# Kernel tuning notes

Measured on AMD Instinct MI355X. Metric: run time of the kernel, lower is better.

Reference implementation:

```python
import jax, jax.numpy as jnp
import numpy as np

S, B, H = 2048, 1, 1024
N_HEADS = 16
HEAD_DIM = H // N_HEADS
E, K, F = 8, 2, 2048  # experts, top_k, ffn_hidden
EPS = 1e-5


def layernorm(x, w, b):
    mu = jnp.mean(x, axis=-1, keepdims=True)
    var = jnp.mean(jnp.square(x - mu), axis=-1, keepdims=True)
    return (x - mu) * jax.lax.rsqrt(var + EPS) * w + b


def setup_inputs() -> dict:
    key = jax.random.key(0)
    ks = jax.random.split(key, 8)
    std = 0.02
    return {
        "x": jax.random.normal(ks[0], (S, B, H), dtype=jnp.float32),
        "ln1_w": jnp.ones((H,), jnp.float32),
        "ln1_b": jnp.zeros((H,), jnp.float32),
        "in_proj_w": jax.random.normal(ks[1], (3 * H, H), jnp.float32) * std,
        "in_proj_b": jnp.zeros((3 * H,), jnp.float32),
        "out_proj_w": jax.random.normal(ks[2], (H, H), jnp.float32) * std,
        "out_proj_b": jnp.zeros((H,), jnp.float32),
        "ln2_w": jnp.ones((H,), jnp.float32),
        "ln2_b": jnp.zeros((H,), jnp.float32),
        "router_w": jax.random.normal(ks[3], (E, H), jnp.float32) * std,
        "w1": jax.random.normal(ks[4], (E, H, F), jnp.float32) * std,
        "w2": jax.random.normal(ks[5], (E, F, H), jnp.float32) * std,
    }


def reference(x, ln1_w, ln1_b, in_proj_w, in_proj_b, out_proj_w, out_proj_b,
              ln2_w, ln2_b, router_w, w1, w2):
    s, b, h = x.shape
    # ---- causal self-attention (nn.MultiheadAttention math) ----
    hn = layernorm(x, ln1_w, ln1_b)
    qkv = hn @ in_proj_w.T + in_proj_b          # [S,B,3H]
    q, k, v = jnp.split(qkv, 3, axis=-1)
    q = q.reshape(s, b, N_HEADS, HEAD_DIM)
    k = k.reshape(s, b, N_HEADS, HEAD_DIM)
    v = v.reshape(s, b, N_HEADS, HEAD_DIM)
    scores = jnp.einsum('sbnd,tbnd->bnst', q, k) / np.sqrt(HEAD_DIM)
    causal = jnp.tril(jnp.ones((s, s), bool))
    scores = jnp.where(causal[None, None], scores, -jnp.inf)
    probs = jax.nn.softmax(scores, axis=-1)
    attn = jnp.einsum('bnst,tbnd->sbnd', probs, v).reshape(s, b, h)
    attn = attn @ out_proj_w.T + out_proj_b
    x1 = x + attn
    # ---- dMoE FFN: router softmax -> top-k gates -> expert GELU MLP ----
    hn2 = layernorm(x1, ln2_w, ln2_b).reshape(s * b, h)   # tokens [T,H]
    logits = hn2 @ router_w.T                              # [T,E]
    rp = jax.nn.softmax(logits, axis=-1)
    topw, topi = jax.lax.top_k(rp, K)                      # [T,K]
    gates = jnp.sum(jax.nn.one_hot(topi, E, dtype=hn2.dtype) * topw[..., None], axis=1)  # [T,E]
    hmid = jax.nn.gelu(jnp.einsum('th,ehf->tef', hn2, w1), approximate=False)  # [T,E,F]
    y = jnp.einsum('tef,efh->th', hmid * gates[:, :, None], w2)                # [T,H]
    return x1 + y.reshape(s, b, h)
```

## Files before the change

### kernel.cpp

```cpp
#include <hip/hip_runtime.h>

#define SL 2048
#define HID 1024
#define NHEAD 16
#define HD 64
#define NEXP 8
#define FF 2048
#define MAXTILE 40
#define MAXROWS (MAXTILE * 128)
#define CPAD 32

typedef short bf16x8 __attribute__((ext_vector_type(8)));
typedef float f32x4 __attribute__((ext_vector_type(4)));

__device__ __forceinline__ unsigned short f2bf(float f) {
  unsigned u = __builtin_bit_cast(unsigned, f);
  u += 0x7fffu + ((u >> 16) & 1u);
  return (unsigned short)(u >> 16);
}

__device__ __forceinline__ void gload16(const void* g, void* l) {
  __builtin_amdgcn_global_load_lds((const __attribute__((address_space(1))) void*)g,
                                   (__attribute__((address_space(3))) void*)l,
                                   16, 0, 0);
}

__device__ __forceinline__ void xcd_remap(int& bx, int& by) {
  const int nx = gridDim.x;
  const int nwg = nx * gridDim.y;
  const int L = by * nx + bx;
  const int per = nwg >> 3;
  const int Lp = (L & 7) * per + (L >> 3);
  bx = Lp % nx;
  by = Lp / nx;
}

template <int MODE>
__global__ __launch_bounds__(256) void gemm_bt(
    const unsigned short* __restrict__ A, const unsigned short* __restrict__ Bt,
    int M, int N, int Kstride, int Kloop,
    const float* __restrict__ bias,
    float* __restrict__ outf,
    unsigned short* __restrict__ q_out, unsigned short* __restrict__ k_out,
    unsigned short* __restrict__ vt_out)
{
  __shared__ unsigned short Asm[2][128 * 32];
  __shared__ unsigned short Bsm[2][128 * 32];
  int bx = blockIdx.x, by = blockIdx.y;
  xcd_remap(bx, by);
  const int tid = threadIdx.x;
  const int wave = tid >> 6;
  const int lane = tid & 63;
  const int m0 = by * 128;
  const int n0 = bx * 128;
  const int koff = blockIdx.z * Kloop;
  const int wm = (wave >> 1) * 64;
  const int wn = (wave & 1) * 64;

  f32x4 acc[4][4] = {};

  const int srow = tid >> 2;
  const int skoff = (tid & 3) * 8;
  const unsigned short* Ag = A + (size_t)(m0 + srow) * Kstride + koff + skoff;
  const unsigned short* Bg = Bt + (size_t)(n0 + srow) * Kstride + koff + skoff;

  const int la = lane & 15;
  const int lk = (lane >> 4) * 8;

  auto stage = [&](int buf, int k0) {
    gload16(Ag + k0, &Asm[buf][wave * 512]);
    gload16(Ag + (size_t)64 * Kstride + k0, &Asm[buf][2048 + wave * 512]);
    gload16(Bg + k0, &Bsm[buf][wave * 512]);
    gload16(Bg + (size_t)64 * Kstride + k0, &Bsm[buf][2048 + wave * 512]);
  };

  stage(0, 0);
  __syncthreads();
  int cur = 0;
  for (int k0 = 0; k0 < Kloop; k0 += 32) {
    if (k0 + 32 < Kloop) stage(cur ^ 1, k0 + 32);
    bf16x8 af[4], bfr[4];
#pragma unroll
    for (int mt = 0; mt < 4; mt++)
      af[mt] = *reinterpret_cast<const bf16x8*>(&Asm[cur][(wm + mt * 16 + la) * 32 + lk]);
#pragma unroll
    for (int nt = 0; nt < 4; nt++)
      bfr[nt] = *reinterpret_cast<const bf16x8*>(&Bsm[cur][(wn + nt * 16 + la) * 32 + lk]);
#pragma unroll
    for (int mt = 0; mt < 4; mt++)
#pragma unroll
      for (int nt = 0; nt < 4; nt++)
        acc[mt][nt] = __builtin_amdgcn_mfma_f32_16x16x32_bf16(af[mt], bfr[nt], acc[mt][nt], 0, 0, 0);
    __syncthreads();
    cur ^= 1;
  }

  const int lg = lane >> 4;
#pragma unroll
  for (int mt = 0; mt < 4; mt++) {
#pragma unroll
    for (int nt = 0; nt < 4; nt++) {
#pragma unroll
      for (int r = 0; r < 4; r++) {
        const int row = m0 + wm + mt * 16 + lg * 4 + r;
        const int col = n0 + wn + nt * 16 + la;
        float v = acc[mt][nt][r];
        if (MODE == 0) {
          v += bias[col];
          const int hh = (col & 1023) >> 6;
          const int dd = col & 63;
          const unsigned short bv = f2bf(v);
          if (col < 1024)
            q_out[(size_t)hh * SL * HD + (size_t)row * HD + dd] = bv;
          else if (col < 2048)
            k_out[(size_t)hh * SL * HD + (size_t)row * HD + dd] = bv;
          else
            vt_out[(size_t)hh * HD * SL + (size_t)dd * SL + row] = bv;
        } else {
          outf[(size_t)blockIdx.z * SL * HID + (size_t)row * HID + col] = v;
        }
      }
    }
  }
}

__global__ __launch_bounds__(256) void gemm_moe1(
    const unsigned short* __restrict__ A, const unsigned short* __restrict__ w1t,
    const int* __restrict__ perm, const float* __restrict__ gateg,
    const int* __restrict__ texp, const int* __restrict__ trow,
    unsigned short* __restrict__ hmidg)
{
  int bx = blockIdx.x, by = blockIdx.y;
  xcd_remap(bx, by);
  const int e = texp[by];
  if (e < 0) return;
  const int row0 = trow[by];
  __shared__ unsigned short Asm[2][128 * 32];
  __shared__ unsigned short Bsm[2][128 * 32];
  const int tid = threadIdx.x;
  const int wave = tid >> 6;
  const int lane = tid & 63;
  const int n0 = bx * 128;
  const int wm = (wave >> 1) * 64;
  const int wn = (wave & 1) * 64;
  f32x4 acc[4][4] = {};
  const int srow = tid >> 2;
  const int skoff = (tid & 3) * 8;
  const int p0 = perm[row0 + srow];
  const int p1 = perm[row0 + 64 + srow];
  const unsigned short* Ag0 = A + (size_t)(p0 < 0 ? 0 : (p0 >> 1)) * HID + skoff;
  const unsigned short* Ag1 = A + (size_t)(p1 < 0 ? 0 : (p1 >> 1)) * HID + skoff;
  const unsigned short* Bg = w1t + (size_t)e * HID * FF + (size_t)(n0 + srow) * HID + skoff;
  const int la = lane & 15;
  const int lk = (lane >> 4) * 8;

  auto stage = [&](int buf, int k0) {
    gload16(Ag0 + k0, &Asm[buf][wave * 512]);
    gload16(Ag1 + k0, &Asm[buf][2048 + wave * 512]);
    gload16(Bg + k0, &Bsm[buf][wave * 512]);
    gload16(Bg + (size_t)64 * HID + k0, &Bsm[buf][2048 + wave * 512]);
  };

  stage(0, 0);
  __syncthreads();
  int cur = 0;
  for (int k0 = 0; k0 < HID; k0 += 32) {
    if (k0 + 32 < HID) stage(cur ^ 1, k0 + 32);
    bf16x8 af[4], bfr[4];
#pragma unroll
    for (int mt = 0; mt < 4; mt++)
      af[mt] = *reinterpret_cast<const bf16x8*>(&Asm[cur][(wm + mt * 16 + la) * 32 + lk]);
#pragma unroll
    for (int nt = 0; nt < 4; nt++)
      bfr[nt] = *reinterpret_cast<const bf16x8*>(&Bsm[cur][(wn + nt * 16 + la) * 32 + lk]);
#pragma unroll
    for (int mt = 0; mt < 4; mt++)
#pragma unroll
      for (int nt = 0; nt < 4; nt++)
        acc[mt][nt] = __builtin_amdgcn_mfma_f32_16x16x32_bf16(af[mt], bfr[nt], acc[mt][nt], 0, 0, 0);
    __syncthreads();
    cur ^= 1;
  }

  const int lg = lane >> 4;
#pragma unroll
  for (int mt = 0; mt < 4; mt++) {
    float gr[4];
#pragma unroll
    for (int r = 0; r < 4; r++) gr[r] = gateg[row0 + wm + mt * 16 + lg * 4 + r];
#pragma unroll
    for (int nt = 0; nt < 4; nt++) {
#pragma unroll
      for (int r = 0; r < 4; r++) {
        const int grow = row0 + wm + mt * 16 + lg * 4 + r;
        const int col = n0 + wn + nt * 16 + la;
        const float v = acc[mt][nt][r];
        const float g = 0.5f * v * (1.0f + erff(v * 0.70710678118f));
        hmidg[(size_t)grow * FF + col] = f2bf(g * gr[r]);
      }
    }
  }
}

__global__ __launch_bounds__(256) void gemm_moe2(
    const unsigned short* __restrict__ A, const unsigned short* __restrict__ w2t,
    const int* __restrict__ perm,
    const int* __restrict__ texp, const int* __restrict__ trow,
    float* __restrict__ ybuf)
{
  int bx = blockIdx.x, by = blockIdx.y;
  xcd_remap(bx, by);
  const int e = texp[by];
  if (e < 0) return;
  const int row0 = trow[by];
  __shared__ unsigned short Asm[2][128 * 32];
  __shared__ unsigned short Bsm[2][128 * 32];
  const int tid = threadIdx.x;
  const int wave = tid >> 6;
  const int lane = tid & 63;
  const int n0 = bx * 128;
  const int koff = blockIdx.z * (FF / 2);
  const int wm = (wave >> 1) * 64;
  const int wn = (wave & 1) * 64;
  f32x4 acc[4][4] = {};
  const int srow = tid >> 2;
  const int skoff = (tid & 3) * 8;
  const unsigned short* Ag = A + (size_t)(row0 + srow) * FF + koff + skoff;
  const unsigned short* Bg = w2t + (size_t)e * FF * HID + (size_t)(n0 + srow) * FF + koff + skoff;
  const int la = lane & 15;
  const int lk = (lane >> 4) * 8;

  auto stage = [&](int buf, int k0) {
    gload16(Ag + k0, &Asm[buf][wave * 512]);
    gload16(Ag + (size_t)64 * FF + k0, &Asm[buf][2048 + wave * 512]);
    gload16(Bg + k0, &Bsm[buf][wave * 512]);
    gload16(Bg + (size_t)64 * FF + k0, &Bsm[buf][2048 + wave * 512]);
  };

  stage(0, 0);
  __syncthreads();
  int cur = 0;
  for (int k0 = 0; k0 < FF / 2; k0 += 32) {
    if (k0 + 32 < FF / 2) stage(cur ^ 1, k0 + 32);
    bf16x8 af[4], bfr[4];
#pragma unroll
    for (int mt = 0; mt < 4; mt++)
      af[mt] = *reinterpret_cast<const bf16x8*>(&Asm[cur][(wm + mt * 16 + la) * 32 + lk]);
#pragma unroll
    for (int nt = 0; nt < 4; nt++)
      bfr[nt] = *reinterpret_cast<const bf16x8*>(&Bsm[cur][(wn + nt * 16 + la) * 32 + lk]);
#pragma unroll
    for (int mt = 0; mt < 4; mt++)
#pragma unroll
      for (int nt = 0; nt < 4; nt++)
        acc[mt][nt] = __builtin_amdgcn_mfma_f32_16x16x32_bf16(af[mt], bfr[nt], acc[mt][nt], 0, 0, 0);
    __syncthreads();
    cur ^= 1;
  }

  const int lg = lane >> 4;
#pragma unroll
  for (int mt = 0; mt < 4; mt++) {
    int pr[4];
#pragma unroll
    for (int r = 0; r < 4; r++) pr[r] = perm[row0 + wm + mt * 16 + lg * 4 + r];
#pragma unroll
    for (int nt = 0; nt < 4; nt++) {
#pragma unroll
      for (int r = 0; r < 4; r++) {
        const int p = pr[r];
        if (p >= 0) {
          const int col = n0 + wn + nt * 16 + la;
          ybuf[(size_t)(blockIdx.z * 2 + (p & 1)) * SL * HID + (size_t)(p >> 1) * HID + col] =
              acc[mt][nt][r];
        }
      }
    }
  }
}

__global__ __launch_bounds__(256) void ln_kernel(
    const float* __restrict__ x, const float* __restrict__ w, const float* __restrict__ b,
    unsigned short* __restrict__ ob, float* __restrict__ of)
{
  const int row = blockIdx.x;
  const int tid = threadIdx.x;
  const float4 v = *reinterpret_cast<const float4*>(&x[(size_t)row * HID + tid * 4]);
  float s = v.x + v.y + v.z + v.w;
  float q = v.x * v.x + v.y * v.y + v.z * v.z + v.w * v.w;
  for (int off = 32; off > 0; off >>= 1) {
    s += __shfl_down(s, off);
    q += __shfl_down(q, off);
  }
  __shared__ float ps[4], pq[4];
  const int wave = tid >> 6, lane = tid & 63;
  if (lane == 0) { ps[wave] = s; pq[wave] = q; }
  __syncthreads();
  s = ps[0] + ps[1] + ps[2] + ps[3];
  q = pq[0] + pq[1] + pq[2] + pq[3];
  const float mu = s * (1.0f / HID);
  const float inv = rsqrtf(q * (1.0f / HID) - mu * mu + 1e-5f);
  const int i = tid * 4;
  const float4 wv = *reinterpret_cast<const float4*>(&w[i]);
  const float4 bv = *reinterpret_cast<const float4*>(&b[i]);
  const float o0 = (v.x - mu) * inv * wv.x + bv.x;
  const float o1 = (v.y - mu) * inv * wv.y + bv.y;
  const float o2 = (v.z - mu) * inv * wv.z + bv.z;
  const float o3 = (v.w - mu) * inv * wv.w + bv.w;
  ushort4 u; u.x = f2bf(o0); u.y = f2bf(o1); u.z = f2bf(o2); u.w = f2bf(o3);
  *reinterpret_cast<ushort4*>(&ob[(size_t)row * HID + i]) = u;
  if (of) {
    float4 o; o.x = o0; o.y = o1; o.z = o2; o.w = o3;
    *reinterpret_cast<float4*>(&of[(size_t)row * HID + i]) = o;
  }
}

__global__ __launch_bounds__(256) void transpose_bf16(
    const float* __restrict__ in, unsigned short* __restrict__ out, int R, int C)
{
  __shared__ float tile[32][33];
  const size_t base = (size_t)blockIdx.z * R * C;
  const int r0 = blockIdx.y * 32, c0 = blockIdx.x * 32;
  const int tx = threadIdx.x & 31, ty = threadIdx.x >> 5;
#pragma unroll
  for (int j = 0; j < 4; j++)
    tile[ty + j * 8][tx] = in[base + (size_t)(r0 + ty + j * 8) * C + c0 + tx];
  __syncthreads();
#pragma unroll
  for (int j = 0; j < 4; j++)
    out[base + (size_t)(c0 + ty + j * 8) * R + r0 + tx] = f2bf(tile[tx][ty + j * 8]);
}

__global__ __launch_bounds__(256) void conv_bf16(
    const float4* __restrict__ in, ushort4* __restrict__ out, int n4)
{
  const int i = blockIdx.x * 256 + threadIdx.x;
  if (i < n4) {
    const float4 v = in[i];
    ushort4 u; u.x = f2bf(v.x); u.y = f2bf(v.y); u.z = f2bf(v.z); u.w = f2bf(v.w);
    out[i] = u;
  }
}

__global__ __launch_bounds__(256) void router_kernel(
    const float* __restrict__ hn2f, const float* __restrict__ rw,
    int* __restrict__ ti, float* __restrict__ tg, int* __restrict__ cnt)
{
  __shared__ float wlds[NEXP * HID];
  __shared__ int lcnt[NEXP];
  const int tid = threadIdx.x;
#pragma unroll
  for (int i = 0; i < 8; i++)
    *reinterpret_cast<float4*>(&wlds[i * 1024 + tid * 4]) =
        *reinterpret_cast<const float4*>(&rw[i * 1024 + tid * 4]);
  if (tid < NEXP) lcnt[tid] = 0;
  __syncthreads();

  const int wave = tid >> 6, lane = tid & 63;
#pragma unroll 1
  for (int k = 0; k < 4; k++) {
    const int t = blockIdx.x * 16 + wave * 4 + k;
    float4 xr[4];
#pragma unroll
    for (int c = 0; c < 4; c++)
      xr[c] = *reinterpret_cast<const float4*>(&hn2f[(size_t)t * HID + c * 256 + lane * 4]);
    float p[NEXP];
#pragma unroll
    for (int e = 0; e < NEXP; e++) {
      float s = 0.f;
#pragma unroll
      for (int c = 0; c < 4; c++) {
        const float4 wv = *reinterpret_cast<const float4*>(&wlds[e * 1024 + c * 256 + lane * 4]);
        s += xr[c].x * wv.x + xr[c].y * wv.y + xr[c].z * wv.z + xr[c].w * wv.w;
      }
      s += __shfl_xor(s, 32);
      s += __shfl_xor(s, 16);
      s += __shfl_xor(s, 8);
      s += __shfl_xor(s, 4);
      s += __shfl_xor(s, 2);
      s += __shfl_xor(s, 1);
      p[e] = s;
    }
    if (lane == 0) {
      float mx = p[0];
#pragma unroll
      for (int e = 1; e < NEXP; e++) mx = fmaxf(mx, p[e]);
      float Z = 0.f;
#pragma unroll
      for (int e = 0; e < NEXP; e++) { p[e] = expf(p[e] - mx); Z += p[e]; }
      const float invZ = 1.f / Z;
      int i1 = 0;
#pragma unroll
      for (int e = 1; e < NEXP; e++) if (p[e] > p[i1]) i1 = e;
      int i2 = (i1 == 0) ? 1 : 0;
#pragma unroll
      for (int e = 0; e < NEXP; e++) if (e != i1 && p[e] > p[i2]) i2 = e;
      ti[2 * t] = i1; ti[2 * t + 1] = i2;
      tg[2 * t] = p[i1] * invZ; tg[2 * t + 1] = p[i2] * invZ;
      atomicAdd(&lcnt[i1], 1);
      atomicAdd(&lcnt[i2], 1);
    }
  }
  __syncthreads();
  if (tid < NEXP && lcnt[tid] > 0) atomicAdd(&cnt[tid * CPAD], lcnt[tid]);
}

__global__ void scan_kernel(const int* __restrict__ cnt, int* __restrict__ poff,
                            int* __restrict__ texp, int* __restrict__ trow)
{
  if (threadIdx.x == 0 && blockIdx.x == 0) {
    int off = 0, nt = 0;
    for (int e = 0; e < NEXP; e++) {
      poff[e] = off;
      const int c = cnt[e * CPAD];
      const int ntl = (c + 127) >> 7;
      for (int i = 0; i < ntl; i++) { texp[nt] = e; trow[nt] = off + i * 128; nt++; }
      off += ntl * 128;
    }
    for (int i = nt; i < MAXTILE; i++) { texp[i] = -1; trow[i] = 0; }
  }
}

__global__ __launch_bounds__(256) void build_kernel(
    const int* __restrict__ ti, const float* __restrict__ tg,
    const int* __restrict__ poff, int* __restrict__ fill,
    int* __restrict__ perm, float* __restrict__ gateg)
{
  __shared__ int lcnt[NEXP], lbase[NEXP];
  const int tid = threadIdx.x;
  if (tid < NEXP) lcnt[tid] = 0;
  __syncthreads();
  const int t = blockIdx.x * 256 + tid;
  int e0 = ti[2 * t], e1 = ti[2 * t + 1];
  int l0 = atomicAdd(&lcnt[e0], 1);
  int l1 = atomicAdd(&lcnt[e1], 1);
  __syncthreads();
  if (tid < NEXP) lbase[tid] = (lcnt[tid] > 0) ? atomicAdd(&fill[tid * CPAD], lcnt[tid]) : 0;
  __syncthreads();
  int pos0 = poff[e0] + lbase[e0] + l0;
  int pos1 = poff[e1] + lbase[e1] + l1;
  perm[pos0] = 2 * t;
  gateg[pos0] = tg[2 * t];
  perm[pos1] = 2 * t + 1;
  gateg[pos1] = tg[2 * t + 1];
}

__global__ __launch_bounds__(256) void combine_x1(
    const float4* __restrict__ x, const float* __restrict__ bias,
    const float4* __restrict__ p0, const float4* __restrict__ p1,
    float4* __restrict__ x1)
{
  const int i = blockIdx.x * 256 + threadIdx.x;
  const int col = (i * 4) & (HID - 1);
  const float4 bv = *reinterpret_cast<const float4*>(&bias[col]);
  const float4 a = x[i], b = p0[i], c = p1[i];
  float4 o;
  o.x = a.x + bv.x + b.x + c.x;
  o.y = a.y + bv.y + b.y + c.y;
  o.z = a.z + bv.z + b.z + c.z;
  o.w = a.w + bv.w + b.w + c.w;
  x1[i] = o;
}

__global__ __launch_bounds__(256) void final_add(
    const float4* __restrict__ x1, const float4* __restrict__ y0,
    const float4* __restrict__ y1, const float4* __restrict__ y2,
    const float4* __restrict__ y3, float4* __restrict__ out)
{
  const int i = blockIdx.x * 256 + threadIdx.x;
  const float4 a = x1[i], b = y0[i], c = y1[i], d = y2[i], e = y3[i];
  float4 o;
  o.x = a.x + b.x + c.x + d.x + e.x;
  o.y = a.y + b.y + c.y + d.y + e.y;
  o.z = a.z + b.z + c.z + d.z + e.z;
  o.w = a.w + b.w + c.w + d.w + e.w;
  out[i] = o;
}

#define SC2 0.1803368801111204f
__global__ __launch_bounds__(512) void attn_kernel(
    const unsigned short* __restrict__ qb, const unsigned short* __restrict__ kb,
    const unsigned short* __restrict__ vtb, unsigned short* __restrict__ attn)
{
  const int h = blockIdx.y;
  const int tid = threadIdx.x;
  const int wave = tid >> 6, lane = tid & 63;
  const int grp = wave >> 2;
  const int w4 = wave & 3;
  const int la = lane & 15, lg = lane >> 4;
  const int la7 = la & 7;
  __shared__ unsigned short Kt[2][2][64 * 64];
  __shared__ unsigned short Vt[2][2][64 * 64];
  __shared__ unsigned short plds[8 * 16 * 64];
  const unsigned short* qh = qb + (size_t)h * SL * HD;
  const unsigned short* kh = kb + (size_t)h * SL * HD;
  const unsigned short* vh = vtb + (size_t)h * HD * SL;

  const int sr_lo = w4 * 8 + (lane >> 3);
  const int ss = lane & 7;

  auto stageKV = [&](int t, int buf) {
    const int kvb = t * 64;
#pragma unroll
    for (int j = 0; j < 2; j++) {
      const int row = j * 32 + sr_lo;
      const int s = ss ^ (row & 7);
      gload16(kh + (size_t)(kvb + row) * HD + s * 8, &Kt[grp][buf][j * 2048 + w4 * 512]);
      gload16(vh + (size_t)row * SL + kvb + s * 8, &Vt[grp][buf][j * 2048 + w4 * 512]);
    }
  };

  for (int half = 0; half < 2; half++) {
    const int qt = half ? (31 - blockIdx.x) : blockIdx.x;
    const int m0 = qt * 64 + w4 * 16;
    const int T = qt + 1;
    const int S = (T + 1) >> 1;

    bf16x8 aq0 = *reinterpret_cast<const bf16x8*>(&qh[(size_t)(m0 + la) * HD + lg * 8]);
    bf16x8 aq1 = *reinterpret_cast<const bf16x8*>(&qh[(size_t)(m0 + la) * HD + 32 + lg * 8]);

    f32x4 oacc[4] = {};
    float mrow[4] = {-1e30f, -1e30f, -1e30f, -1e30f};
    float lrow[4] = {0.f, 0.f, 0.f, 0.f};

    if (grp < T) stageKV(grp, 0);
    __syncthreads();
    int cur = 0;

    for (int s = 0; s < S; s++) {
      const int tmy = 2 * s + grp;
      if (tmy + 2 < T) stageKV(tmy + 2, cur ^ 1);
      if (tmy < T) {
        const int kv0 = tmy * 64;
        const unsigned short* Kb = Kt[grp][cur];
        const unsigned short* Vb = Vt[grp][cur];

        f32x4 sac[4] = {};
#pragma unroll
        for (int nt = 0; nt < 4; nt++) {
          const int row = nt * 16 + la;
          bf16x8 b0 = *reinterpret_cast<const bf16x8*>(&Kb[row * 64 + ((lg ^ la7) << 3)]);
          bf16x8 b1 = *reinterpret_cast<const bf16x8*>(&Kb[row * 64 + (((4 + lg) ^ la7) << 3)]);
          sac[nt] = __builtin_amdgcn_mfma_f32_16x16x32_bf16(aq0, b0, sac[nt], 0, 0, 0);
          sac[nt] = __builtin_amdgcn_mfma_f32_16x16x32_bf16(aq1, b1, sac[nt], 0, 0, 0);
        }
        float sv[4][4];
        const bool diag = (tmy == qt);
#pragma unroll
        for (int nt = 0; nt < 4; nt++)
#pragma unroll
          for (int r = 0; r < 4; r++) {
            float xs = sac[nt][r] * SC2;
            if (diag && (kv0 + nt * 16 + la) > (m0 + lg * 4 + r)) xs = -1e30f;
            sv[nt][r] = xs;
          }
        float alpha[4];
#pragma unroll
        for (int r = 0; r < 4; r++) {
          float tm = fmaxf(fmaxf(sv[0][r], sv[1][r]), fmaxf(sv[2][r], sv[3][r]));
          tm = fmaxf(tm, __shfl_xor(tm, 1));
          tm = fmaxf(tm, __shfl_xor(tm, 2));
          tm = fmaxf(tm, __shfl_xor(tm, 4));
          tm = fmaxf(tm, __shfl_xor(tm, 8));
          const float mn = fmaxf(mrow[r], tm);
          alpha[r] = exp2f(mrow[r] - mn);
          float rs = 0.f;
#pragma unroll
          for (int nt = 0; nt < 4; nt++) {
            const float pe = exp2f(sv[nt][r] - mn);
            sv[nt][r] = pe;
            rs += pe;
          }
          rs += __shfl_xor(rs, 1);
          rs += __shfl_xor(rs, 2);
          rs += __shfl_xor(rs, 4);
          rs += __shfl_xor(rs, 8);
          lrow[r] = lrow[r] * alpha[r] + rs;
          mrow[r] = mn;
        }
#pragma unroll
        for (int dt = 0; dt < 4; dt++)
#pragma unroll
          for (int r = 0; r < 4; r++) oacc[dt][r] *= alpha[r];

#pragma unroll
        for (int nt = 0; nt < 4; nt++)
#pragma unroll
          for (int r = 0; r < 4; r++) {
            const int row = lg * 4 + r;
            const int slot = nt * 2 + (la >> 3);
            plds[wave * 1024 + row * 64 + ((slot ^ (row & 7)) << 3) + la7] = f2bf(sv[nt][r]);
          }
        asm volatile("s_waitcnt lgkmcnt(0)" ::: "memory");
        bf16x8 pa0 = *reinterpret_cast<const bf16x8*>(&plds[wave * 1024 + la * 64 + ((lg ^ la7) << 3)]);
        bf16x8 pa1 = *reinterpret_cast<const bf16x8*>(&plds[wave * 1024 + la * 64 + (((4 + lg) ^ la7) << 3)]);
#pragma unroll
        for (int dt = 0; dt < 4; dt++) {
          const int row = dt * 16 + la;
          bf16x8 v0 = *reinterpret_cast<const bf16x8*>(&Vb[row * 64 + ((lg ^ la7) << 3)]);
          bf16x8 v1 = *reinterpret_cast<const bf16x8*>(&Vb[row * 64 + (((4 + lg) ^ la7) << 3)]);
          oacc[dt] = __builtin_amdgcn_mfma_f32_16x16x32_bf16(pa0, v0, oacc[dt], 0, 0, 0);
          oacc[dt] = __builtin_amdgcn_mfma_f32_16x16x32_bf16(pa1, v1, oacc[dt], 0, 0, 0);
        }
      }
      __syncthreads();
      cur ^= 1;
    }

    float* xb = (float*)&Kt[0][0][0];
    float* mlb = (float*)&Vt[0][0][0];
    if (grp == 1) {
#pragma unroll
      for (int dt = 0; dt < 4; dt++)
#pragma unroll
        for (int r = 0; r < 4; r++)
          xb[w4 * 1024 + (lg * 4 + r) * 64 + dt * 16 + la] = oacc[dt][r];
      if (la == 0) {
#pragma unroll
        for (int r = 0; r < 4; r++) {
          mlb[w4 * 32 + (lg * 4 + r) * 2] = mrow[r];
          mlb[w4 * 32 + (lg * 4 + r) * 2 + 1] = lrow[r];
        }
      }
    }
    __syncthreads();
    if (grp == 0) {
#pragma unroll
      for (int r = 0; r < 4; r++) {
        const int row = lg * 4 + r;
        const float m1 = mlb[w4 * 32 + row * 2];
        const float l1 = mlb[w4 * 32 + row * 2 + 1];
        const float mm = fmaxf(mrow[r], m1);
        const float a0 = exp2f(mrow[r] - mm);
        const float a1 = exp2f(m1 - mm);
        const float linv = 1.0f / (lrow[r] * a0 + l1 * a1);
#pragma unroll
        for (int dt = 0; dt < 4; dt++) {
          const float o1 = xb[w4 * 1024 + row * 64 + dt * 16 + la];
          const float o = (oacc[dt][r] * a0 + o1 * a1) * linv;
          attn[(size_t)(m0 + row) * HID + h * HD + dt * 16 + la] = f2bf(o);
        }
      }
    }
    __syncthreads();
  }
}

extern "C" void kernel_launch(void* const* d_in, const int* in_sizes, int n_in,
                              void* d_out, int out_size, void* d_ws, size_t ws_size,
                              hipStream_t stream)
{
  const float* x          = (const float*)d_in[0];
  const float* ln1_w      = (const float*)d_in[1];
  const float* ln1_b      = (const float*)d_in[2];
  const float* in_proj_w  = (const float*)d_in[3];
  const float* in_proj_b  = (const float*)d_in[4];
  const float* out_proj_w = (const float*)d_in[5];
  const float* out_proj_b = (const float*)d_in[6];
  const float* ln2_w      = (const float*)d_in[7];
  const float* ln2_b      = (const float*)d_in[8];
  const float* router_w   = (const float*)d_in[9];
  const float* w1         = (const float*)d_in[10];
  const float* w2         = (const float*)d_in[11];
  float* out = (float*)d_out;

  char* ws = (char*)d_ws;
  size_t off = 0;
  auto alloc = [&](size_t bytes) -> void* {
    void* p = ws + off;
    off += (bytes + 255) & ~(size_t)255;
    return p;
  };
  unsigned short* hn_b   = (unsigned short*)alloc((size_t)SL * HID * 2);
  unsigned short* ipw_b  = (unsigned short*)alloc((size_t)3 * HID * HID * 2);
  unsigned short* opw_b  = (unsigned short*)alloc((size_t)HID * HID * 2);
  unsigned short* qb     = (unsigned short*)alloc((size_t)SL * HID * 2);
  unsigned short* kb     = (unsigned short*)alloc((size_t)SL * HID * 2);
  unsigned short* vtb    = (unsigned short*)alloc((size_t)SL * HID * 2);
  unsigned short* attn_b = (unsigned short*)alloc((size_t)SL * HID * 2);
  float*          x1     = (float*)alloc((size_t)SL * HID * 4);
  float*          pbuf   = (float*)alloc((size_t)2 * SL * HID * 4);
  unsigned short* hn2_b  = (unsigned short*)alloc((size_t)SL * HID * 2);
  float*          hn2_f  = (float*)alloc((size_t)SL * HID * 4);
  unsigned short* w1t    = (unsigned short*)alloc((size_t)NEXP * HID * FF * 2);
  unsigned short* w2t    = (unsigned short*)alloc((size_t)NEXP * HID * FF * 2);
  unsigned short* hmidg  = (unsigned short*)alloc((size_t)MAXROWS * FF * 2);
  float*          ybuf   = (float*)alloc((size_t)4 * SL * HID * 4);
  int*            ti     = (int*)alloc((size_t)SL * 2 * 4);
  float*          tg     = (float*)alloc((size_t)SL * 2 * 4);
  int*            perm   = (int*)alloc((size_t)MAXROWS * 4);
  float*          gateg  = (float*)alloc((size_t)MAXROWS * 4);
  int*            cnt    = (int*)alloc(NEXP * CPAD * 4);
  int*            fill   = (int*)alloc(NEXP * CPAD * 4);
  int*            poff   = (int*)alloc(64 * 4);
  int*            texp   = (int*)alloc(64 * 4);
  int*            trow   = (int*)alloc(64 * 4);

  const dim3 blk(256);

  hipMemsetAsync(cnt, 0, NEXP * CPAD * 4, stream);
  hipMemsetAsync(fill, 0, NEXP * CPAD * 4, stream);
  hipMemsetAsync(perm, 0xFF, (size_t)MAXROWS * 4, stream);
  hipMemsetAsync(gateg, 0, (size_t)MAXROWS * 4, stream);

  conv_bf16<<<(3 * HID * HID / 4 + 255) / 256, blk, 0, stream>>>(
      (const float4*)in_proj_w, (ushort4*)ipw_b, 3 * HID * HID / 4);
  conv_bf16<<<(HID * HID / 4 + 255) / 256, blk, 0, stream>>>(
      (const float4*)out_proj_w, (ushort4*)opw_b, HID * HID / 4);
  transpose_bf16<<<dim3(FF / 32, HID / 32, NEXP), blk, 0, stream>>>(w1, w1t, HID, FF);
  transpose_bf16<<<dim3(HID / 32, FF / 32, NEXP), blk, 0, stream>>>(w2, w2t, FF, HID);

  ln_kernel<<<SL, blk, 0, stream>>>(x, ln1_w, ln1_b, hn_b, nullptr);

  gemm_bt<0><<<dim3(3 * HID / 128, SL / 128), blk, 0, stream>>>(
      hn_b, ipw_b, SL, 3 * HID, HID, HID,
      in_proj_b, nullptr, qb, kb, vtb);

  attn_kernel<<<dim3(16, NHEAD), dim3(512), 0, stream>>>(qb, kb, vtb, attn_b);

  gemm_bt<2><<<dim3(HID / 128, SL / 128, 2), blk, 0, stream>>>(
      attn_b, opw_b, SL, HID, HID, HID / 2,
      nullptr, pbuf, nullptr, nullptr, nullptr);
  combine_x1<<<SL * HID / 1024, blk, 0, stream>>>(
      (const float4*)x, out_proj_b, (const float4*)pbuf,
      (const float4*)(pbuf + (size_t)SL * HID), (float4*)x1);

  ln_kernel<<<SL, blk, 0, stream>>>(x1, ln2_w, ln2_b, hn2_b, hn2_f);

  router_kernel<<<SL / 16, blk, 0, stream>>>(hn2_f, router_w, ti, tg, cnt);
  scan_kernel<<<1, 64, 0, stream>>>(cnt, poff, texp, trow);
  build_kernel<<<SL / 256, blk, 0, stream>>>(ti, tg, poff, fill, perm, gateg);

  gemm_moe1<<<dim3(FF / 128, MAXTILE), blk, 0, stream>>>(
      hn2_b, w1t, perm, gateg, texp, trow, hmidg);
  gemm_moe2<<<dim3(HID / 128, MAXTILE, 2), blk, 0, stream>>>(
      hmidg, w2t, perm, texp, trow, ybuf);

  final_add<<<SL * HID / 1024, blk, 0, stream>>>(
      (const float4*)x1, (const float4*)ybuf,
      (const float4*)(ybuf + (size_t)SL * HID),
      (const float4*)(ybuf + (size_t)2 * SL * HID),
      (const float4*)(ybuf + (size_t)3 * SL * HID),
      (float4*)out);
}
```

Before: 284.5 us.

## Transpose attention MFMA operands for per-lane softmax rows and widen weight transpose

The attention kernel swaps the MFMA A/B operands so each lane holds one query row. The softmax max and sum then need only two cross-lane shuffles, and the output rescale is skipped when no row max increases in the wave. P is packed to bf16 pairs with v_cvt_pk_bf16_f32 into a padded LDS layout, and the output is written as ushort4. Separately, the weight transpose kernel moves to 64x64 tiles with float4 loads and ushort4 stores, cutting memory transactions in the per-call weight conversion at the cost of more LDS per block.

```diff
diff --git a/kernel.cpp b/kernel.cpp
--- a/kernel.cpp
+++ b/kernel.cpp
@@ -12,6 +12,7 @@
 
 typedef short bf16x8 __attribute__((ext_vector_type(8)));
 typedef float f32x4 __attribute__((ext_vector_type(4)));
+typedef unsigned u32x4 __attribute__((ext_vector_type(4)));
 
 __device__ __forceinline__ unsigned short f2bf(float f) {
   unsigned u = __builtin_bit_cast(unsigned, f);
@@ -318,17 +319,27 @@
 __global__ __launch_bounds__(256) void transpose_bf16(
     const float* __restrict__ in, unsigned short* __restrict__ out, int R, int C)
 {
-  __shared__ float tile[32][33];
+  __shared__ float t[64][65];
   const size_t base = (size_t)blockIdx.z * R * C;
-  const int r0 = blockIdx.y * 32, c0 = blockIdx.x * 32;
-  const int tx = threadIdx.x & 31, ty = threadIdx.x >> 5;
-#pragma unroll
-  for (int j = 0; j < 4; j++)
-    tile[ty + j * 8][tx] = in[base + (size_t)(r0 + ty + j * 8) * C + c0 + tx];
-  __syncthreads();
-#pragma unroll
-  for (int j = 0; j < 4; j++)
-    out[base + (size_t)(c0 + ty + j * 8) * R + r0 + tx] = f2bf(tile[tx][ty + j * 8]);
+  const int r0 = blockIdx.y * 64, c0 = blockIdx.x * 64;
+  const int tid = threadIdx.x;
+#pragma unroll
+  for (int it = 0; it < 4; it++) {
+    const int idx = it * 256 + tid;
+    const int r = idx >> 4, c4 = (idx & 15) * 4;
+    const float4 v = *reinterpret_cast<const float4*>(&in[base + (size_t)(r0 + r) * C + c0 + c4]);
+    t[r][c4] = v.x; t[r][c4 + 1] = v.y; t[r][c4 + 2] = v.z; t[r][c4 + 3] = v.w;
+  }
+  __syncthreads();
+#pragma unroll
+  for (int it = 0; it < 4; it++) {
+    const int idx = it * 256 + tid;
+    const int c = idx >> 4, r4 = (idx & 15) * 4;
+    ushort4 u;
+    u.x = f2bf(t[r4][c]); u.y = f2bf(t[r4 + 1][c]);
+    u.z = f2bf(t[r4 + 2][c]); u.w = f2bf(t[r4 + 3][c]);
+    *reinterpret_cast<ushort4*>(&out[base + (size_t)(c0 + c) * R + r0 + r4]) = u;
+  }
 }
 
 __global__ __launch_bounds__(256) void conv_bf16(
@@ -478,6 +489,7 @@
 }
 
 #define SC2 0.1803368801111204f
+#define PPITCH 20
 __global__ __launch_bounds__(512) void attn_kernel(
     const unsigned short* __restrict__ qb, const unsigned short* __restrict__ kb,
     const unsigned short* __restrict__ vtb, unsigned short* __restrict__ attn)
@@ -491,10 +503,11 @@
   const int la7 = la & 7;
   __shared__ unsigned short Kt[2][2][64 * 64];
   __shared__ unsigned short Vt[2][2][64 * 64];
-  __shared__ unsigned short plds[8 * 16 * 64];
+  __shared__ unsigned plds[8 * 32 * PPITCH];
   const unsigned short* qh = qb + (size_t)h * SL * HD;
   const unsigned short* kh = kb + (size_t)h * SL * HD;
   const unsigned short* vh = vtb + (size_t)h * HD * SL;
+  unsigned* pu = &plds[wave * 32 * PPITCH];
 
   const int sr_lo = w4 * 8 + (lane >> 3);
   const int ss = lane & 7;
@@ -515,13 +528,13 @@
     const int m0 = qt * 64 + w4 * 16;
     const int T = qt + 1;
     const int S = (T + 1) >> 1;
+    const int q = m0 + la;
 
     bf16x8 aq0 = *reinterpret_cast<const bf16x8*>(&qh[(size_t)(m0 + la) * HD + lg * 8]);
     bf16x8 aq1 = *reinterpret_cast<const bf16x8*>(&qh[(size_t)(m0 + la) * HD + 32 + lg * 8]);
 
     f32x4 oacc[4] = {};
-    float mrow[4] = {-1e30f, -1e30f, -1e30f, -1e30f};
-    float lrow[4] = {0.f, 0.f, 0.f, 0.f};
+    float mrun = -1e30f, lrun = 0.f;
 
     if (grp < T) stageKV(grp, 0);
     __syncthreads();
@@ -541,8 +554,8 @@
           const int row = nt * 16 + la;
           bf16x8 b0 = *reinterpret_cast<const bf16x8*>(&Kb[row * 64 + ((lg ^ la7) << 3)]);
           bf16x8 b1 = *reinterpret_cast<const bf16x8*>(&Kb[row * 64 + (((4 + lg) ^ la7) << 3)]);
-          sac[nt] = __builtin_amdgcn_mfma_f32_16x16x32_bf16(aq0, b0, sac[nt], 0, 0, 0);
-          sac[nt] = __builtin_amdgcn_mfma_f32_16x16x32_bf16(aq1, b1, sac[nt], 0, 0, 0);
+          sac[nt] = __builtin_amdgcn_mfma_f32_16x16x32_bf16(b0, aq0, sac[nt], 0, 0, 0);
+          sac[nt] = __builtin_amdgcn_mfma_f32_16x16x32_bf16(b1, aq1, sac[nt], 0, 0, 0);
         }
         float sv[4][4];
         const bool diag = (tmy == qt);
@@ -551,56 +564,64 @@
 #pragma unroll
           for (int r = 0; r < 4; r++) {
             float xs = sac[nt][r] * SC2;
-            if (diag && (kv0 + nt * 16 + la) > (m0 + lg * 4 + r)) xs = -1e30f;
+            if (diag && (kv0 + nt * 16 + lg * 4 + r) > q) xs = -1e30f;
             sv[nt][r] = xs;
           }
-        float alpha[4];
-#pragma unroll
-        for (int r = 0; r < 4; r++) {
-          float tm = fmaxf(fmaxf(sv[0][r], sv[1][r]), fmaxf(sv[2][r], sv[3][r]));
-          tm = fmaxf(tm, __shfl_xor(tm, 1));
-          tm = fmaxf(tm, __shfl_xor(tm, 2));
-          tm = fmaxf(tm, __shfl_xor(tm, 4));
-          tm = fmaxf(tm, __shfl_xor(tm, 8));
-          const float mn = fmaxf(mrow[r], tm);
-          alpha[r] = exp2f(mrow[r] - mn);
-          float rs = 0.f;
-#pragma unroll
-          for (int nt = 0; nt < 4; nt++) {
+        float pm = fmaxf(fmaxf(sv[0][0], sv[0][1]), fmaxf(sv[0][2], sv[0][3]));
+#pragma unroll
+        for (int nt = 1; nt < 4; nt++)
+          pm = fmaxf(pm, fmaxf(fmaxf(sv[nt][0], sv[nt][1]), fmaxf(sv[nt][2], sv[nt][3])));
+        pm = fmaxf(pm, __shfl_xor(pm, 16));
+        pm = fmaxf(pm, __shfl_xor(pm, 32));
+        const float mn = fmaxf(mrun, pm);
+        float rs = 0.f;
+#pragma unroll
+        for (int nt = 0; nt < 4; nt++)
+#pragma unroll
+          for (int r = 0; r < 4; r++) {
             const float pe = exp2f(sv[nt][r] - mn);
             sv[nt][r] = pe;
             rs += pe;
           }
-          rs += __shfl_xor(rs, 1);
-          rs += __shfl_xor(rs, 2);
-          rs += __shfl_xor(rs, 4);
-          rs += __shfl_xor(rs, 8);
-          lrow[r] = lrow[r] * alpha[r] + rs;
-          mrow[r] = mn;
+        rs += __shfl_xor(rs, 16);
+        rs += __shfl_xor(rs, 32);
+        if (__ballot(pm > mrun) != 0ULL) {
+          const float al = exp2f(mrun - mn);
+#pragma unroll
+          for (int dt = 0; dt < 4; dt++)
+#pragma unroll
+            for (int r = 0; r < 4; r++) oacc[dt][r] *= al;
+          lrun = lrun * al + rs;
+          mrun = mn;
+        } else {
+          lrun += rs;
         }
 #pragma unroll
-        for (int dt = 0; dt < 4; dt++)
-#pragma unroll
-          for (int r = 0; r < 4; r++) oacc[dt][r] *= alpha[r];
-
-#pragma unroll
         for (int nt = 0; nt < 4; nt++)
 #pragma unroll
-          for (int r = 0; r < 4; r++) {
-            const int row = lg * 4 + r;
-            const int slot = nt * 2 + (la >> 3);
-            plds[wave * 1024 + row * 64 + ((slot ^ (row & 7)) << 3) + la7] = f2bf(sv[nt][r]);
+          for (int rp = 0; rp < 2; rp++) {
+            unsigned pk;
+            asm("v_cvt_pk_bf16_f32 %0, %1, %2"
+                : "=v"(pk) : "v"(sv[nt][rp * 2]), "v"(sv[nt][rp * 2 + 1]));
+            pu[(nt * 8 + lg * 2 + rp) * PPITCH + la] = pk;
           }
         asm volatile("s_waitcnt lgkmcnt(0)" ::: "memory");
-        bf16x8 pa0 = *reinterpret_cast<const bf16x8*>(&plds[wave * 1024 + la * 64 + ((lg ^ la7) << 3)]);
-        bf16x8 pa1 = *reinterpret_cast<const bf16x8*>(&plds[wave * 1024 + la * 64 + (((4 + lg) ^ la7) << 3)]);
+        __builtin_amdgcn_sched_barrier(0);
+        u32x4 w0, w1;
+#pragma unroll
+        for (int jj = 0; jj < 4; jj++) {
+          w0[jj] = pu[(lg * 4 + jj) * PPITCH + la];
+          w1[jj] = pu[(16 + lg * 4 + jj) * PPITCH + la];
+        }
+        const bf16x8 pa0 = __builtin_bit_cast(bf16x8, w0);
+        const bf16x8 pa1 = __builtin_bit_cast(bf16x8, w1);
 #pragma unroll
         for (int dt = 0; dt < 4; dt++) {
           const int row = dt * 16 + la;
           bf16x8 v0 = *reinterpret_cast<const bf16x8*>(&Vb[row * 64 + ((lg ^ la7) << 3)]);
           bf16x8 v1 = *reinterpret_cast<const bf16x8*>(&Vb[row * 64 + (((4 + lg) ^ la7) << 3)]);
-          oacc[dt] = __builtin_amdgcn_mfma_f32_16x16x32_bf16(pa0, v0, oacc[dt], 0, 0, 0);
-          oacc[dt] = __builtin_amdgcn_mfma_f32_16x16x32_bf16(pa1, v1, oacc[dt], 0, 0, 0);
+          oacc[dt] = __builtin_amdgcn_mfma_f32_16x16x32_bf16(v0, pa0, oacc[dt], 0, 0, 0);
+          oacc[dt] = __builtin_amdgcn_mfma_f32_16x16x32_bf16(v1, pa1, oacc[dt], 0, 0, 0);
         }
       }
       __syncthreads();
@@ -614,32 +635,29 @@
       for (int dt = 0; dt < 4; dt++)
 #pragma unroll
         for (int r = 0; r < 4; r++)
-          xb[w4 * 1024 + (lg * 4 + r) * 64 + dt * 16 + la] = oacc[dt][r];
-      if (la == 0) {
-#pragma unroll
-        for (int r = 0; r < 4; r++) {
-          mlb[w4 * 32 + (lg * 4 + r) * 2] = mrow[r];
-          mlb[w4 * 32 + (lg * 4 + r) * 2 + 1] = lrow[r];
-        }
+          xb[w4 * 1024 + (dt * 16 + lg * 4 + r) * 16 + la] = oacc[dt][r];
+      if (lg == 0) {
+        mlb[w4 * 32 + la * 2] = mrun;
+        mlb[w4 * 32 + la * 2 + 1] = lrun;
       }
     }
     __syncthreads();
     if (grp == 0) {
-#pragma unroll
-      for (int r = 0; r < 4; r++) {
-        const int row = lg * 4 + r;
-        const float m1 = mlb[w4 * 32 + row * 2];
-        const float l1 = mlb[w4 * 32 + row * 2 + 1];
-        const float mm = fmaxf(mrow[r], m1);
-        const float a0 = exp2f(mrow[r] - mm);
-        const float a1 = exp2f(m1 - mm);
-        const float linv = 1.0f / (lrow[r] * a0 + l1 * a1);
-#pragma unroll
-        for (int dt = 0; dt < 4; dt++) {
-          const float o1 = xb[w4 * 1024 + row * 64 + dt * 16 + la];
-          const float o = (oacc[dt][r] * a0 + o1 * a1) * linv;
-          attn[(size_t)(m0 + row) * HID + h * HD + dt * 16 + la] = f2bf(o);
-        }
+      const float m1 = mlb[w4 * 32 + la * 2];
+      const float l1 = mlb[w4 * 32 + la * 2 + 1];
+      const float mm = fmaxf(mrun, m1);
+      const float a0 = exp2f(mrun - mm);
+      const float a1 = exp2f(m1 - mm);
+      const float linv = 1.0f / (lrun * a0 + l1 * a1);
+#pragma unroll
+      for (int dt = 0; dt < 4; dt++) {
+        ushort4 u;
+        float o0 = (oacc[dt][0] * a0 + xb[w4 * 1024 + (dt * 16 + lg * 4 + 0) * 16 + la] * a1) * linv;
+        float o1 = (oacc[dt][1] * a0 + xb[w4 * 1024 + (dt * 16 + lg * 4 + 1) * 16 + la] * a1) * linv;
+        float o2 = (oacc[dt][2] * a0 + xb[w4 * 1024 + (dt * 16 + lg * 4 + 2) * 16 + la] * a1) * linv;
+        float o3 = (oacc[dt][3] * a0 + xb[w4 * 1024 + (dt * 16 + lg * 4 + 3) * 16 + la] * a1) * linv;
+        u.x = f2bf(o0); u.y = f2bf(o1); u.z = f2bf(o2); u.w = f2bf(o3);
+        *reinterpret_cast<ushort4*>(&attn[(size_t)q * HID + h * HD + dt * 16 + lg * 4]) = u;
       }
     }
     __syncthreads();
@@ -707,8 +725,8 @@
       (const float4*)in_proj_w, (ushort4*)ipw_b, 3 * HID * HID / 4);
   conv_bf16<<<(HID * HID / 4 + 255) / 256, blk, 0, stream>>>(
       (const float4*)out_proj_w, (ushort4*)opw_b, HID * HID / 4);
-  transpose_bf16<<<dim3(FF / 32, HID / 32, NEXP), blk, 0, stream>>>(w1, w1t, HID, FF);
-  transpose_bf16<<<dim3(HID / 32, FF / 32, NEXP), blk, 0, stream>>>(w2, w2t, FF, HID);
+  transpose_bf16<<<dim3(FF / 64, HID / 64, NEXP), blk, 0, stream>>>(w1, w1t, HID, FF);
+  transpose_bf16<<<dim3(HID / 64, FF / 64, NEXP), blk, 0, stream>>>(w2, w2t, FF, HID);
 
   ln_kernel<<<SL, blk, 0, stream>>>(x, ln1_w, ln1_b, hn_b, nullptr);
 
```

Result: faster. 272.3 us (-4.3%).
